# Kernel tuning notes

Hardware: AMD Instinct MI355X
Metric: run time of the kernel (lower is better)

Reference implementation:

```python
import jax, jax.numpy as jnp
import numpy as np

NUM_ITERS = 3

def squash(s, axis=-1):
    # standard capsule squash: ||s||^2/(1+||s||^2) * s/||s||
    sq = jnp.sum(s * s, axis=axis, keepdims=True)
    norm = jnp.sqrt(sq)
    return (sq / (1.0 + sq)) * (s / norm)

def setup_inputs() -> dict:
    key = jax.random.key(0)
    kx, kw = jax.random.split(key)
    B, I, k, l, O = 512, 1152, 8, 16, 7
    x = jax.random.normal(kx, (B, I, k), dtype=jnp.float32)
    w = jax.random.normal(kw, (I, k, l, O), dtype=jnp.float32)
    return {"x": x, "w": w}

def reference(x, w):
    # x: [B, I, k]; w: [I, k, l, O]
    u_hat = jnp.einsum('BIk,IklO->BIlO', x, w)            # [B, I, l, O]
    I, _, l, _ = w.shape
    b_ij = jnp.zeros((I, l), dtype=u_hat.dtype)
    v_j = None
    for _ in range(NUM_ITERS):
        c_ij = jax.nn.softmax(b_ij, axis=0)               # softmax over I
        s_j = jnp.einsum('Il,BIlO->BlO', c_ij, u_hat)     # [B, l, O]
        v_j = jnp.transpose(squash(s_j), (0, 2, 1))       # [B, O, l]
        u_vj = jnp.einsum('BOl,BIlO->BIl', v_j, u_hat).mean(axis=0)  # [I, l]
        b_ij = b_ij + u_vj
    return v_j
```

## Files before the change

### kernel.cpp

```cpp
#include <hip/hip_runtime.h>
#include <hip/hip_bf16.h>


#define NB 512
#define NI 1152
#define NLO 112
#define NIK 9216
#define KSPLIT 48
#define SPART 57344

typedef __attribute__((ext_vector_type(8))) short bf16x8;
typedef __attribute__((ext_vector_type(4))) float f32x4;

__device__ __forceinline__ ushort f2bf(float f) {
    __hip_bfloat16 h = __float2bfloat16(f);
    return *(ushort*)&h;
}

__global__ void softmax_col(const float* __restrict__ b, float* __restrict__ c) {
    int l = blockIdx.x;
    int t = threadIdx.x;
    __shared__ float red[256];
    float m = -1e30f;
    for (int i = t; i < NI; i += 256) m = fmaxf(m, b[i * 16 + l]);
    red[t] = m; __syncthreads();
    for (int s = 128; s > 0; s >>= 1) {
        if (t < s) red[t] = fmaxf(red[t], red[t + s]);
        __syncthreads();
    }
    m = red[0]; __syncthreads();
    float sum = 0.f;
    for (int i = t; i < NI; i += 256) sum += expf(b[i * 16 + l] - m);
    red[t] = sum; __syncthreads();
    for (int s = 128; s > 0; s >>= 1) {
        if (t < s) red[t] += red[t + s];
        __syncthreads();
    }
    float inv = 1.0f / red[0];
    for (int i = t; i < NI; i += 256) c[i * 16 + l] = expf(b[i * 16 + l] - m) * inv;
}

__global__ __launch_bounds__(256) void conv_x(const float* __restrict__ x,
                                              ushort* __restrict__ xbf,
                                              ushort* __restrict__ xT) {
    __shared__ ushort tile[64][68];
    int kg = blockIdx.x % 144, bg = blockIdx.x / 144;
    int k0 = kg * 64, b0 = bg * 64;
    int t = threadIdx.x;
    for (int e = t; e < 1024; e += 256) {
        int r = e >> 4, c4 = (e & 15) * 4;
        float4 f = *(const float4*)&x[(size_t)(b0 + r) * NIK + k0 + c4];
        ushort4 u = { f2bf(f.x), f2bf(f.y), f2bf(f.z), f2bf(f.w) };
        *(ushort4*)&xbf[(size_t)(b0 + r) * NIK + k0 + c4] = u;
        tile[r][c4] = u.x; tile[r][c4 + 1] = u.y; tile[r][c4 + 2] = u.z; tile[r][c4 + 3] = u.w;
    }
    __syncthreads();
    for (int e = t; e < 1024; e += 256) {
        int kr = e >> 4, c4 = (e & 15) * 4;
        ushort4 u = { tile[c4][kr], tile[c4 + 1][kr], tile[c4 + 2][kr], tile[c4 + 3][kr] };
        *(ushort4*)&xT[(size_t)(k0 + kr) * NB + b0 + c4] = u;
    }
}

__global__ __launch_bounds__(256) void conv_wc(const float* __restrict__ c,
                                               const float* __restrict__ w,
                                               ushort* __restrict__ wcT) {
    __shared__ ushort tile[NLO][66];
    __shared__ float cs[128];
    int ik0 = blockIdx.x * 64;
    int t = threadIdx.x;
    if (t < 128) cs[t] = c[(size_t)(ik0 >> 3) * 16 + t];
    __syncthreads();
    for (int e = t; e < 7168; e += 256) {
        int ikl = e / NLO, lo = e - ikl * NLO;
        int il = ((ikl >> 3) << 4) + lo / 7;
        tile[lo][ikl] = f2bf(cs[il] * w[(size_t)(ik0 + ikl) * NLO + lo]);
    }
    __syncthreads();
    for (int e = t; e < 7168; e += 256) {
        int lo = e >> 6, ikl = e & 63;
        wcT[(size_t)lo * NIK + ik0 + ikl] = tile[lo][ikl];
    }
}

__global__ __launch_bounds__(256) void s_gemm(const ushort* __restrict__ xbf,
                                              const ushort* __restrict__ wcT,
                                              float* __restrict__ part) {
    int wid = blockIdx.x * 4 + (threadIdx.x >> 6);
    int lane = threadIdx.x & 63;
    int mt = wid & 31;
    int kc = wid >> 5;
    int b0 = mt * 16, k0 = kc * 192;
    int row = lane & 15, quad = lane >> 4;
    const ushort* ap = xbf + (size_t)(b0 + row) * NIK + k0 + quad * 8;
    const ushort* bp = wcT + (size_t)row * NIK + k0 + quad * 8;
    f32x4 acc[7];
    #pragma unroll
    for (int nt = 0; nt < 7; ++nt) acc[nt] = (f32x4){0.f, 0.f, 0.f, 0.f};
    for (int ks = 0; ks < 6; ++ks) {
        bf16x8 a = *(const bf16x8*)(ap + ks * 32);
        #pragma unroll
        for (int nt = 0; nt < 7; ++nt) {
            bf16x8 bfr = *(const bf16x8*)(bp + (size_t)nt * 16 * NIK + ks * 32);
            acc[nt] = __builtin_amdgcn_mfma_f32_16x16x32_bf16(a, bfr, acc[nt], 0, 0, 0);
        }
    }
    float* pp = part + (size_t)kc * SPART + (size_t)(b0 + quad * 4) * NLO + row;
    #pragma unroll
    for (int nt = 0; nt < 7; ++nt)
        #pragma unroll
        for (int r = 0; r < 4; ++r)
            pp[(size_t)r * NLO + nt * 16] = acc[nt][r];
}

__global__ void squash_k(const float* __restrict__ part, ushort* __restrict__ vT,
                         float* __restrict__ out, int write_out) {
    int b = blockIdx.x;
    int t = threadIdx.x;
    __shared__ float sh[NLO];
    __shared__ float fac[16];
    float sv = 0.f;
    if (t < NLO) {
        const float* p = part + (size_t)b * NLO + t;
        #pragma unroll 8
        for (int kc = 0; kc < KSPLIT; ++kc) sv += p[(size_t)kc * SPART];
        sh[t] = sv;
    }
    __syncthreads();
    if (t < 16) {
        float sq = 0.f;
        #pragma unroll
        for (int o = 0; o < 7; ++o) { float e = sh[t * 7 + o]; sq += e * e; }
        fac[t] = sqrtf(sq) / (1.0f + sq);
    }
    __syncthreads();
    if (t < NLO) {
        int l = t / 7, o = t - l * 7;
        float vv = sv * fac[l];
        vT[(size_t)(o * 16 + l) * NB + b] = f2bf(vv);
        if (write_out) out[(size_t)b * NLO + o * 16 + l] = vv;
    }
}

__global__ __launch_bounds__(256) void g_fused(const ushort* __restrict__ xT,
                                               const ushort* __restrict__ vT,
                                               const float* __restrict__ w,
                                               float* __restrict__ bij) {
    int wid = blockIdx.x * 4 + (threadIdx.x >> 6);
    int lane = threadIdx.x & 63;
    int m0 = wid * 16;
    int row = lane & 15, quad = lane >> 4;
    const ushort* ap = xT + (size_t)(m0 + row) * NB + quad * 8;
    const ushort* bp = vT + (size_t)row * NB + quad * 8;
    f32x4 acc[7];
    #pragma unroll
    for (int nt = 0; nt < 7; ++nt) acc[nt] = (f32x4){0.f, 0.f, 0.f, 0.f};
    for (int ks = 0; ks < 16; ++ks) {
        bf16x8 a = *(const bf16x8*)(ap + ks * 32);
        #pragma unroll
        for (int nt = 0; nt < 7; ++nt) {
            bf16x8 bfr = *(const bf16x8*)(bp + (size_t)nt * 16 * NB + ks * 32);
            acc[nt] = __builtin_amdgcn_mfma_f32_16x16x32_bf16(a, bfr, acc[nt], 0, 0, 0);
        }
    }
    float S = 0.f;
    #pragma unroll
    for (int r = 0; r < 4; ++r) {
        int ik = m0 + quad * 4 + r;
        const float* wr = w + (size_t)ik * NLO + row * 7;
        float p = 0.f;
        #pragma unroll
        for (int o = 0; o < 7; ++o) p += wr[o] * acc[o][r];
        S += p;
    }
    float Sp = __shfl_down(S, 16);
    if ((quad & 1) == 0) {
        int i = (m0 >> 3) + (quad >> 1);
        bij[(size_t)i * 16 + row] += (S + Sp) * (1.0f / 512.0f);
    }
}

extern "C" void kernel_launch(void* const* d_in, const int* in_sizes, int n_in,
                              void* d_out, int out_size, void* d_ws, size_t ws_size,
                              hipStream_t stream) {
    const float* x = (const float*)d_in[0];
    const float* w = (const float*)d_in[1];
    float* out = (float*)d_out;
    float* ws = (float*)d_ws;
    float*  f_b    = ws;
    float*  f_c    = f_b + 18432;
    float*  f_part = f_c + 18432;
    ushort* xbf    = (ushort*)(f_part + (size_t)KSPLIT * SPART);
    ushort* xT     = xbf + (size_t)NB * NIK;
    ushort* wcT    = xT + (size_t)NIK * NB;
    ushort* vT     = wcT + (size_t)NLO * NIK;
    hipMemsetAsync(f_b, 0, 18432 * sizeof(float), stream);
    conv_x<<<1152, 256, 0, stream>>>(x, xbf, xT);
    for (int it = 0; it < 3; ++it) {
        softmax_col<<<16, 256, 0, stream>>>(f_b, f_c);
        conv_wc<<<144, 256, 0, stream>>>(f_c, w, wcT);
        s_gemm<<<384, 256, 0, stream>>>(xbf, wcT, f_part);
        squash_k<<<512, 128, 0, stream>>>(f_part, vT, out, it == 2 ? 1 : 0);
        if (it < 2) g_fused<<<144, 256, 0, stream>>>(xT, vT, w, f_b);
    }
}
```

Baseline: 199.8 us.

## Fuse softmax into weight conversion, split GEMM K further, merge prep kernels

Folds the column softmax into the weighted-W conversion kernel: each block recomputes the softmax statistics redundantly and iteration 0 uses a constant uniform coefficient. The x conversion and the first W conversion are merged into one launch, and the memset is dropped. The S GEMM K-split is doubled to 96 for more parallelism, squash processes two batches per block, and the G GEMM is split over the batch into two partial b buffers that the next softmax sums. This removes several launches and raises occupancy, at the cost of redundant softmax reductions over all of b in every block and more partial-sum traffic in squash.

```diff
diff --git a/kernel.cpp b/kernel.cpp
--- a/kernel.cpp
+++ b/kernel.cpp
@@ -6,7 +6,7 @@
 #define NI 1152
 #define NLO 112
 #define NIK 9216
-#define KSPLIT 48
+#define KSPLIT 96
 #define SPART 57344
 
 typedef __attribute__((ext_vector_type(8))) short bf16x8;
@@ -17,34 +17,63 @@
     return *(ushort*)&h;
 }
 
-__global__ void softmax_col(const float* __restrict__ b, float* __restrict__ c) {
-    int l = blockIdx.x;
+__device__ __forceinline__ void smaxwc_body(const float* __restrict__ bij0,
+                                            const float* __restrict__ bij1,
+                                            const float* __restrict__ w,
+                                            ushort* __restrict__ wcT,
+                                            int ik0, int it0flag) {
+    __shared__ ushort tile[NLO][66];
+    __shared__ float cs[128];
+    __shared__ float red[256];
+    __shared__ float m_l[16], inv_l[16];
     int t = threadIdx.x;
-    __shared__ float red[256];
-    float m = -1e30f;
-    for (int i = t; i < NI; i += 256) m = fmaxf(m, b[i * 16 + l]);
-    red[t] = m; __syncthreads();
-    for (int s = 128; s > 0; s >>= 1) {
-        if (t < s) red[t] = fmaxf(red[t], red[t + s]);
+    if (!it0flag) {
+        float mx = -1e30f;
+        for (int e = t; e < NI * 16; e += 256) mx = fmaxf(mx, bij0[e] + bij1[e]);
+        red[t] = mx; __syncthreads();
+        if (t < 16) {
+            float m = red[t];
+            #pragma unroll
+            for (int j = 1; j < 16; ++j) m = fmaxf(m, red[t + j * 16]);
+            m_l[t] = m;
+        }
         __syncthreads();
-    }
-    m = red[0]; __syncthreads();
-    float sum = 0.f;
-    for (int i = t; i < NI; i += 256) sum += expf(b[i * 16 + l] - m);
-    red[t] = sum; __syncthreads();
-    for (int s = 128; s > 0; s >>= 1) {
-        if (t < s) red[t] += red[t + s];
+        float m = m_l[t & 15];
+        float sm = 0.f;
+        for (int e = t; e < NI * 16; e += 256) sm += expf(bij0[e] + bij1[e] - m);
+        red[t] = sm; __syncthreads();
+        if (t < 16) {
+            float s = 0.f;
+            #pragma unroll
+            for (int j = 0; j < 16; ++j) s += red[t + j * 16];
+            inv_l[t] = 1.0f / s;
+        }
         __syncthreads();
-    }
-    float inv = 1.0f / red[0];
-    for (int i = t; i < NI; i += 256) c[i * 16 + l] = expf(b[i * 16 + l] - m) * inv;
-}
-
-__global__ __launch_bounds__(256) void conv_x(const float* __restrict__ x,
-                                              ushort* __restrict__ xbf,
-                                              ushort* __restrict__ xT) {
+        if (t < 128) {
+            int i = (ik0 >> 3) + (t >> 4), l = t & 15;
+            cs[t] = expf(bij0[i * 16 + l] + bij1[i * 16 + l] - m_l[l]) * inv_l[l];
+        }
+    } else {
+        if (t < 128) cs[t] = 1.0f / 1152.0f;
+    }
+    __syncthreads();
+    for (int e = t; e < 7168; e += 256) {
+        int ikl = e / NLO, lo = e - ikl * NLO;
+        int il = ((ikl >> 3) << 4) + lo / 7;
+        tile[lo][ikl] = f2bf(cs[il] * w[(size_t)(ik0 + ikl) * NLO + lo]);
+    }
+    __syncthreads();
+    for (int e = t; e < 7168; e += 256) {
+        int lo = e >> 6, ikl = e & 63;
+        wcT[(size_t)lo * NIK + ik0 + ikl] = tile[lo][ikl];
+    }
+}
+
+__device__ __forceinline__ void conv_x_body(const float* __restrict__ x,
+                                            ushort* __restrict__ xbf,
+                                            ushort* __restrict__ xT, int bid) {
     __shared__ ushort tile[64][68];
-    int kg = blockIdx.x % 144, bg = blockIdx.x / 144;
+    int kg = bid % 144, bg = bid / 144;
     int k0 = kg * 64, b0 = bg * 64;
     int t = threadIdx.x;
     for (int e = t; e < 1024; e += 256) {
@@ -62,25 +91,19 @@
     }
 }
 
-__global__ __launch_bounds__(256) void conv_wc(const float* __restrict__ c,
-                                               const float* __restrict__ w,
-                                               ushort* __restrict__ wcT) {
-    __shared__ ushort tile[NLO][66];
-    __shared__ float cs[128];
-    int ik0 = blockIdx.x * 64;
-    int t = threadIdx.x;
-    if (t < 128) cs[t] = c[(size_t)(ik0 >> 3) * 16 + t];
-    __syncthreads();
-    for (int e = t; e < 7168; e += 256) {
-        int ikl = e / NLO, lo = e - ikl * NLO;
-        int il = ((ikl >> 3) << 4) + lo / 7;
-        tile[lo][ikl] = f2bf(cs[il] * w[(size_t)(ik0 + ikl) * NLO + lo]);
-    }
-    __syncthreads();
-    for (int e = t; e < 7168; e += 256) {
-        int lo = e >> 6, ikl = e & 63;
-        wcT[(size_t)lo * NIK + ik0 + ikl] = tile[lo][ikl];
-    }
+__global__ __launch_bounds__(256) void prep0(const float* __restrict__ x,
+                                             ushort* __restrict__ xbf,
+                                             ushort* __restrict__ xT,
+                                             const float* __restrict__ w,
+                                             ushort* __restrict__ wcT) {
+    if (blockIdx.x < 1152) conv_x_body(x, xbf, xT, blockIdx.x);
+    else smaxwc_body(nullptr, nullptr, w, wcT, (blockIdx.x - 1152) * 64, 1);
+}
+
+__global__ __launch_bounds__(256) void smaxwc(const float* __restrict__ bijp,
+                                              const float* __restrict__ w,
+                                              ushort* __restrict__ wcT) {
+    smaxwc_body(bijp, bijp + NI * 16, w, wcT, blockIdx.x * 64, 0);
 }
 
 __global__ __launch_bounds__(256) void s_gemm(const ushort* __restrict__ xbf,
@@ -90,14 +113,15 @@
     int lane = threadIdx.x & 63;
     int mt = wid & 31;
     int kc = wid >> 5;
-    int b0 = mt * 16, k0 = kc * 192;
+    int b0 = mt * 16, k0 = kc * 96;
     int row = lane & 15, quad = lane >> 4;
     const ushort* ap = xbf + (size_t)(b0 + row) * NIK + k0 + quad * 8;
     const ushort* bp = wcT + (size_t)row * NIK + k0 + quad * 8;
     f32x4 acc[7];
     #pragma unroll
     for (int nt = 0; nt < 7; ++nt) acc[nt] = (f32x4){0.f, 0.f, 0.f, 0.f};
-    for (int ks = 0; ks < 6; ++ks) {
+    #pragma unroll
+    for (int ks = 0; ks < 3; ++ks) {
         bf16x8 a = *(const bf16x8*)(ap + ks * 32);
         #pragma unroll
         for (int nt = 0; nt < 7; ++nt) {
@@ -113,30 +137,32 @@
             pp[(size_t)r * NLO + nt * 16] = acc[nt][r];
 }
 
-__global__ void squash_k(const float* __restrict__ part, ushort* __restrict__ vT,
-                         float* __restrict__ out, int write_out) {
-    int b = blockIdx.x;
-    int t = threadIdx.x;
-    __shared__ float sh[NLO];
-    __shared__ float fac[16];
+__global__ __launch_bounds__(256) void squash_k(const float* __restrict__ part,
+                                                ushort* __restrict__ vT,
+                                                float* __restrict__ out, int write_out) {
+    int half = threadIdx.x >> 7;
+    int b = blockIdx.x * 2 + half;
+    int t = threadIdx.x & 127;
+    __shared__ float sh[2][NLO];
+    __shared__ float fac[2][16];
     float sv = 0.f;
     if (t < NLO) {
         const float* p = part + (size_t)b * NLO + t;
         #pragma unroll 8
         for (int kc = 0; kc < KSPLIT; ++kc) sv += p[(size_t)kc * SPART];
-        sh[t] = sv;
+        sh[half][t] = sv;
     }
     __syncthreads();
     if (t < 16) {
         float sq = 0.f;
         #pragma unroll
-        for (int o = 0; o < 7; ++o) { float e = sh[t * 7 + o]; sq += e * e; }
-        fac[t] = sqrtf(sq) / (1.0f + sq);
+        for (int o = 0; o < 7; ++o) { float e = sh[half][t * 7 + o]; sq += e * e; }
+        fac[half][t] = sqrtf(sq) / (1.0f + sq);
     }
     __syncthreads();
     if (t < NLO) {
         int l = t / 7, o = t - l * 7;
-        float vv = sv * fac[l];
+        float vv = sv * fac[half][l];
         vT[(size_t)(o * 16 + l) * NB + b] = f2bf(vv);
         if (write_out) out[(size_t)b * NLO + o * 16 + l] = vv;
     }
@@ -145,17 +171,19 @@
 __global__ __launch_bounds__(256) void g_fused(const ushort* __restrict__ xT,
                                                const ushort* __restrict__ vT,
                                                const float* __restrict__ w,
-                                               float* __restrict__ bij) {
+                                               float* __restrict__ bijp, int accum) {
     int wid = blockIdx.x * 4 + (threadIdx.x >> 6);
     int lane = threadIdx.x & 63;
-    int m0 = wid * 16;
+    int half = wid & 1;
+    int m0 = (wid >> 1) * 16;
+    int kb0 = half * 256;
     int row = lane & 15, quad = lane >> 4;
-    const ushort* ap = xT + (size_t)(m0 + row) * NB + quad * 8;
-    const ushort* bp = vT + (size_t)row * NB + quad * 8;
+    const ushort* ap = xT + (size_t)(m0 + row) * NB + kb0 + quad * 8;
+    const ushort* bp = vT + (size_t)row * NB + kb0 + quad * 8;
     f32x4 acc[7];
     #pragma unroll
     for (int nt = 0; nt < 7; ++nt) acc[nt] = (f32x4){0.f, 0.f, 0.f, 0.f};
-    for (int ks = 0; ks < 16; ++ks) {
+    for (int ks = 0; ks < 8; ++ks) {
         bf16x8 a = *(const bf16x8*)(ap + ks * 32);
         #pragma unroll
         for (int nt = 0; nt < 7; ++nt) {
@@ -176,7 +204,9 @@
     float Sp = __shfl_down(S, 16);
     if ((quad & 1) == 0) {
         int i = (m0 >> 3) + (quad >> 1);
-        bij[(size_t)i * 16 + row] += (S + Sp) * (1.0f / 512.0f);
+        float val = (S + Sp) * (1.0f / 512.0f);
+        float* dst = bijp + (size_t)half * (NI * 16) + i * 16 + row;
+        *dst = accum ? (*dst + val) : val;
     }
 }
 
@@ -187,20 +217,17 @@
     const float* w = (const float*)d_in[1];
     float* out = (float*)d_out;
     float* ws = (float*)d_ws;
-    float*  f_b    = ws;
-    float*  f_c    = f_b + 18432;
-    float*  f_part = f_c + 18432;
+    float*  f_bijp = ws;
+    float*  f_part = f_bijp + 2 * NI * 16;
     ushort* xbf    = (ushort*)(f_part + (size_t)KSPLIT * SPART);
     ushort* xT     = xbf + (size_t)NB * NIK;
     ushort* wcT    = xT + (size_t)NIK * NB;
     ushort* vT     = wcT + (size_t)NLO * NIK;
-    hipMemsetAsync(f_b, 0, 18432 * sizeof(float), stream);
-    conv_x<<<1152, 256, 0, stream>>>(x, xbf, xT);
+    prep0<<<1296, 256, 0, stream>>>(x, xbf, xT, w, wcT);
     for (int it = 0; it < 3; ++it) {
-        softmax_col<<<16, 256, 0, stream>>>(f_b, f_c);
-        conv_wc<<<144, 256, 0, stream>>>(f_c, w, wcT);
-        s_gemm<<<384, 256, 0, stream>>>(xbf, wcT, f_part);
-        squash_k<<<512, 128, 0, stream>>>(f_part, vT, out, it == 2 ? 1 : 0);
-        if (it < 2) g_fused<<<144, 256, 0, stream>>>(xT, vT, w, f_b);
-    }
-}
+        if (it > 0) smaxwc<<<144, 256, 0, stream>>>(f_bijp, w, wcT);
+        s_gemm<<<768, 256, 0, stream>>>(xbf, wcT, f_part);
+        squash_k<<<256, 256, 0, stream>>>(f_part, vT, out, it == 2 ? 1 : 0);
+        if (it < 2) g_fused<<<288, 256, 0, stream>>>(xT, vT, w, f_bijp, it);
+    }
+}
```

New measurement: 233.4 us. 1.17x slower.
